# Optimization experiments

Measured on AMD Instinct MI355X. Metric: run time of the kernel, lower is better.

The kernel has to match this reference:

```python
import jax, jax.numpy as jnp
import numpy as np

N_NODES = 50000
N_EDGES = 800000
NFEAT = 128
NHID = 128
NCLASS = 10
N_GRAPHS = 256


def _segment_mean(vals, idx, num):
    # scatter-mean: sum then divide by count, count clamped to 1 (PyG 'mean' semantics)
    s = jax.ops.segment_sum(vals, idx, num_segments=num)
    c = jax.ops.segment_sum(jnp.ones((vals.shape[0], 1), vals.dtype), idx, num_segments=num)
    return s / jnp.maximum(c, 1.0)


def _graph_conv(x, src, dst, W_n, b_n, W_s):
    # gather x at source nodes, scatter-mean into destination nodes
    agg = _segment_mean(x[src], dst, x.shape[0])          # [N, C_in]
    return agg @ W_n.T + b_n + x @ W_s.T                  # [N, C_out]


def setup_inputs() -> dict:
    key = jax.random.key(0)
    ks = jax.random.split(key, 12)

    def lin_w(k, o, i):
        return (jax.random.uniform(k, (o, i), jnp.float32) * 2.0 - 1.0) / np.sqrt(i)

    x = jax.random.normal(ks[0], (N_NODES, NFEAT), jnp.float32)
    edge_index = jax.random.randint(ks[1], (2, N_EDGES), 0, N_NODES, dtype=jnp.int32)
    batch = jnp.sort(jax.random.randint(ks[2], (N_NODES,), 0, N_GRAPHS, dtype=jnp.int32))

    return {
        "x": x,
        "edge_index": edge_index,
        "batch": batch,
        "W1n": lin_w(ks[3], NHID, NFEAT), "b1": jnp.zeros((NHID,), jnp.float32), "W1s": lin_w(ks[4], NHID, NFEAT),
        "W2n": lin_w(ks[5], NHID, NHID), "b2": jnp.zeros((NHID,), jnp.float32), "W2s": lin_w(ks[6], NHID, NHID),
        "W3n": lin_w(ks[7], NHID, NHID), "b3": jnp.zeros((NHID,), jnp.float32), "W3s": lin_w(ks[8], NHID, NHID),
        "Wlin": lin_w(ks[9], NCLASS, NHID), "blin": jnp.zeros((NCLASS,), jnp.float32),
    }


def reference(x, edge_index, batch, W1n, b1, W1s, W2n, b2, W2s, W3n, b3, W3s, Wlin, blin):
    src, dst = edge_index[0], edge_index[1]
    h = jax.nn.relu(_graph_conv(x, src, dst, W1n, b1, W1s))
    h = jax.nn.relu(_graph_conv(h, src, dst, W2n, b2, W2s))
    h = jax.nn.relu(_graph_conv(h, src, dst, W3n, b3, W3s))
    g = _segment_mean(h, batch, N_GRAPHS)                 # global_mean_pool -> [G, NHID]
    # dropout is identity at inference
    logits = g @ Wlin.T + blin                            # [G, NCLASS]
    return jax.nn.log_softmax(logits, axis=1)
```

## Files before the change

kernel.cpp:

```cpp
#include <hip/hip_runtime.h>
#include <hip/hip_bf16.h>

#define NNODES 50000
#define NEDGES 800000
#define NFEAT 128
#define NHID 128
#define NCLASS 10
#define NGRAPHS 256

#define NB 391
#define HB 128

typedef __attribute__((ext_vector_type(8))) short short8;
typedef __attribute__((ext_vector_type(4))) short short4v;
typedef __attribute__((ext_vector_type(4))) float floatx4;

__device__ __forceinline__ float bf2f(unsigned short u) {
    union { unsigned i; float f; } c; c.i = ((unsigned)u) << 16; return c.f;
}
__device__ __forceinline__ unsigned short f2bf(float f) {
    union { float f; unsigned i; } c; c.f = f;
    unsigned x = c.i;
    unsigned r = (x + 0x7fffu + ((x >> 16) & 1u)) >> 16;
    return (unsigned short)r;
}
__device__ __forceinline__ float blo(unsigned v) { return bf2f((unsigned short)(v & 0xffffu)); }
__device__ __forceinline__ float bhi(unsigned v) { return bf2f((unsigned short)(v >> 16)); }

__device__ __forceinline__ void gload_lds16(const void* gsrc, void* ldst) {
    __builtin_amdgcn_global_load_lds(
        (const __attribute__((address_space(1))) void*)gsrc,
        (__attribute__((address_space(3))) void*)ldst, 16, 0, 0);
}

__global__ __launch_bounds__(256) void k_hist(const int* __restrict__ dst,
                                              int* __restrict__ hist) {
    __shared__ int lh[NB];
    int tid = threadIdx.x;
    for (int b = tid; b < NB; b += 256) lh[b] = 0;
    __syncthreads();
    for (int i = blockIdx.x * 256 + tid; i < NEDGES; i += HB * 256)
        atomicAdd(&lh[dst[i] >> 7], 1);
    __syncthreads();
    for (int b = tid; b < NB; b += 256) hist[b * HB + blockIdx.x] = lh[b];
}

__global__ __launch_bounds__(512) void k_scan2(const int* __restrict__ hist,
                                               int* __restrict__ base,
                                               int* __restrict__ boff,
                                               int* __restrict__ row_ptr,
                                               const int* __restrict__ batch,
                                               int* __restrict__ gstart) {
    __shared__ int tot[NB];
    int tid = threadIdx.x;
    int wid = tid >> 6, l = tid & 63;
    if (tid <= NGRAPHS) {
        int lo = 0, hi = NNODES;
        while (lo < hi) { int mid = (lo + hi) >> 1; if (batch[mid] < tid) lo = mid + 1; else hi = mid; }
        gstart[tid] = lo;
    }
    for (int q = wid; q < NB; q += 8) {
        int h0 = hist[q * HB + l];
        int h1 = hist[q * HB + 64 + l];
        int s0 = h0, s1 = h1;
        #pragma unroll
        for (int d = 1; d < 64; d <<= 1) {
            int y0 = __shfl_up(s0, d);
            int y1 = __shfl_up(s1, d);
            if (l >= d) { s0 += y0; s1 += y1; }
        }
        int t0 = __shfl(s0, 63);
        base[q * HB + l] = s0 - h0;
        base[q * HB + 64 + l] = s1 - h1 + t0;
        if (l == 63) tot[q] = t0 + s1;
    }
    __syncthreads();
    if (wid == 0) {
        int carry = 0;
        #pragma unroll
        for (int c = 0; c < (NB + 63) / 64; ++c) {
            int i = c * 64 + l;
            int v = (i < NB) ? tot[i] : 0;
            int s = v;
            #pragma unroll
            for (int d = 1; d < 64; d <<= 1) { int y = __shfl_up(s, d); if (l >= d) s += y; }
            if (i < NB) boff[i] = carry + s - v;
            carry += __shfl(s, 63);
        }
        if (l == 0) { boff[NB] = carry; row_ptr[NNODES] = carry; }
    }
}

__global__ __launch_bounds__(256) void k_scatter(const int* __restrict__ src,
                                                 const int* __restrict__ dst,
                                                 const int* __restrict__ base,
                                                 const int* __restrict__ boff,
                                                 unsigned* __restrict__ ebuf) {
    __shared__ int cur[NB];
    int tid = threadIdx.x;
    for (int b = tid; b < NB; b += 256) cur[b] = boff[b] + base[b * HB + blockIdx.x];
    __syncthreads();
    for (int i = blockIdx.x * 256 + tid; i < NEDGES; i += HB * 256) {
        int d = dst[i];
        int bin = d >> 7;
        int pos = atomicAdd(&cur[bin], 1);
        ebuf[pos] = (unsigned)src[i] | ((unsigned)(d & 127) << 16);
    }
}

__global__ __launch_bounds__(256) void k_bcsr(const unsigned* __restrict__ ebuf,
                                              const int* __restrict__ boff,
                                              int* __restrict__ row_ptr,
                                              int* __restrict__ esrc) {
    __shared__ int deg[128];
    __shared__ int curs[128];
    int tid = threadIdx.x;
    int b = blockIdx.x;
    int s = boff[b], e = boff[b + 1];
    if (tid < 128) deg[tid] = 0;
    __syncthreads();
    for (int i = s + tid; i < e; i += 256) atomicAdd(&deg[ebuf[i] >> 16], 1);
    __syncthreads();
    if (tid == 0) {
        int run = s;
        for (int i = 0; i < 128; ++i) { curs[i] = run; run += deg[i]; }
    }
    __syncthreads();
    if (tid < 128) {
        int node = b * 128 + tid;
        if (node < NNODES) row_ptr[node] = curs[tid];
    }
    __syncthreads();
    for (int i = s + tid; i < e; i += 256) {
        unsigned pk = ebuf[i];
        int pos = atomicAdd(&curs[pk >> 16], 1);
        esrc[pos] = (int)(pk & 0xffffu);
    }
}

__global__ void k_cvt(const float* __restrict__ x,
                      const float* __restrict__ w0, const float* __restrict__ w1,
                      const float* __restrict__ w2, const float* __restrict__ w3,
                      const float* __restrict__ w4, const float* __restrict__ w5,
                      unsigned short* __restrict__ xb, unsigned short* __restrict__ wb) {
    int gid = blockIdx.x * blockDim.x + threadIdx.x;
    const int NX4 = NNODES * NFEAT / 4;
    const floatx4* srcv;
    short4v* dstv;
    if (gid < NX4) {
        srcv = (const floatx4*)x + gid;
        dstv = (short4v*)xb + gid;
    } else {
        int j = gid - NX4;
        if (j >= 6 * 4096) return;
        int m = j >> 12;
        int o4 = j & 4095;
        const float* w = (m == 0) ? w0 : (m == 1) ? w1 : (m == 2) ? w2
                       : (m == 3) ? w3 : (m == 4) ? w4 : w5;
        srcv = (const floatx4*)w + o4;
        dstv = (short4v*)wb + (m * 4096 + o4);
    }
    floatx4 v = *srcv;
    short4v o;
    #pragma unroll
    for (int k = 0; k < 4; ++k) o[k] = (short)f2bf(v[k]);
    *dstv = o;
}

__global__ __launch_bounds__(512, 4) void k_layer(const unsigned short* __restrict__ feat,
                                                  const int* __restrict__ row_ptr,
                                                  const int* __restrict__ esrc,
                                                  const unsigned short* __restrict__ Bn,
                                                  const unsigned short* __restrict__ Bs,
                                                  const float* __restrict__ bias,
                                                  unsigned short* __restrict__ out) {
    __shared__ __align__(16) unsigned short ldsA[2][8192];
    int w = threadIdx.x >> 6;
    int l = threadIdx.x & 63;
    int r = l & 15;
    int gk = l >> 4;
    int m0 = blockIdx.x * 64;

    {
        int c = l & 15;
        #pragma unroll
        for (int is = 0; is < 2; ++is) {
            int row = is * 32 + (w << 2) + (l >> 4);
            int nrow = m0 + row; if (nrow >= NNODES) nrow = NNODES - 1;
            gload_lds16(feat + (size_t)nrow * 128 + ((c ^ (row & 15)) << 3),
                        &ldsA[1][(is * 32 + (w << 2)) * 128]);
        }
    }

    const unsigned* feat32 = (const unsigned*)feat;
    unsigned* A1 = (unsigned*)&ldsA[0][0];
    #pragma unroll 1
    for (int i = 0; i < 8; ++i) {
        int row = (w << 3) + i;
        int n = m0 + row;
        float a0 = 0.f, a1 = 0.f;
        int nb = 0;
        if (n < NNODES) {
            int beg = row_ptr[n];
            nb = row_ptr[n + 1] - beg;
            for (int base = 0; base < nb; base += 64) {
                int rem = nb - base;
                int cnt = rem < 64 ? rem : 64;
                int myidx = (l < cnt) ? esrc[beg + base + l] : 0;
                int j = 0;
                for (; j + 4 <= cnt; j += 4) {
                    int s0 = __shfl(myidx, j);
                    int s1 = __shfl(myidx, j + 1);
                    int s2 = __shfl(myidx, j + 2);
                    int s3 = __shfl(myidx, j + 3);
                    unsigned v0 = feat32[s0 * 64 + l];
                    unsigned v1 = feat32[s1 * 64 + l];
                    unsigned v2 = feat32[s2 * 64 + l];
                    unsigned v3 = feat32[s3 * 64 + l];
                    a0 += (blo(v0) + blo(v1)) + (blo(v2) + blo(v3));
                    a1 += (bhi(v0) + bhi(v1)) + (bhi(v2) + bhi(v3));
                }
                for (; j < cnt; ++j) {
                    int s0 = __shfl(myidx, j);
                    unsigned v0 = feat32[s0 * 64 + l];
                    a0 += blo(v0);
                    a1 += bhi(v0);
                }
            }
        }
        float inv = 1.0f / (float)max(nb, 1);
        unsigned o = ((unsigned)f2bf(a0 * inv)) | (((unsigned)f2bf(a1 * inv)) << 16);
        int c = l >> 2;
        A1[row * 64 + ((c ^ (row & 15)) << 2) + (l & 3)] = o;
    }

    short8 bf[8];
    #pragma unroll
    for (int kt = 0; kt < 8; ++kt) {
        const unsigned short* Bbase = (kt < 4 ? Bn : Bs);
        bf[kt] = *(const short8*)(Bbase + (w * 16 + r) * 128 + (kt & 3) * 32 + gk * 8);
    }
    int o = w * 16 + r;
    float bias_v = bias[o];

    __syncthreads();

    #pragma unroll
    for (int t = 0; t < 4; ++t) {
        short8 af[8];
        #pragma unroll
        for (int kt = 0; kt < 8; ++kt) {
            int half = kt >> 2;
            int Cr = ((((kt & 3) << 2) + gk) ^ r) << 3;
            af[kt] = *(const short8*)(&ldsA[half][(t * 16 + r) * 128 + Cr]);
        }
        floatx4 acc = {0.f, 0.f, 0.f, 0.f};
        #pragma unroll
        for (int kt = 0; kt < 8; ++kt)
            acc = __builtin_amdgcn_mfma_f32_16x16x32_bf16(af[kt], bf[kt], acc, 0, 0, 0);
        #pragma unroll
        for (int j = 0; j < 4; ++j) {
            int mrow = m0 + t * 16 + gk * 4 + j;
            if (mrow < NNODES) {
                float v = acc[j] + bias_v;
                v = v > 0.f ? v : 0.f;
                out[mrow * 128 + o] = f2bf(v);
            }
        }
    }
}

__global__ __launch_bounds__(256) void k_pool(const unsigned short* __restrict__ h,
                                              const int* __restrict__ gstart,
                                              float* __restrict__ part) {
    int g = blockIdx.x >> 3;
    int c = blockIdx.x & 7;
    int s = gstart[g], e = gstart[g + 1];
    int len = e - s;
    int cs = s + (len * c) / 8;
    int ce = s + (len * (c + 1)) / 8;
    int w = threadIdx.x >> 6;
    int l = threadIdx.x & 63;
    const unsigned* h32 = (const unsigned*)h;
    float a0 = 0.f, a1 = 0.f;
    for (int n = cs + w; n < ce; n += 4) {
        unsigned v = h32[n * 64 + l];
        a0 += blo(v);
        a1 += bhi(v);
    }
    __shared__ float red[4][128];
    red[w][2 * l] = a0;
    red[w][2 * l + 1] = a1;
    __syncthreads();
    if (w == 0) {
        float r0 = (red[0][2 * l] + red[1][2 * l]) + (red[2][2 * l] + red[3][2 * l]);
        float r1 = (red[0][2 * l + 1] + red[1][2 * l + 1]) + (red[2][2 * l + 1] + red[3][2 * l + 1]);
        float* dst = part + (size_t)(g * 8 + c) * 128;
        dst[2 * l] = r0;
        dst[2 * l + 1] = r1;
    }
}

__global__ __launch_bounds__(128) void k_head(const float* __restrict__ part,
                                              const int* __restrict__ gstart,
                                              const float* __restrict__ Wlin,
                                              const float* __restrict__ blin,
                                              float* __restrict__ out) {
    int gi = blockIdx.x;
    __shared__ float gl[128];
    __shared__ float lg[NCLASS];
    int t = threadIdx.x;
    float s = 0.f;
    #pragma unroll
    for (int c = 0; c < 8; ++c) s += part[(size_t)(gi * 8 + c) * 128 + t];
    int len = gstart[gi + 1] - gstart[gi];
    gl[t] = s / (float)max(len, 1);
    __syncthreads();
    if (t < NCLASS) {
        float a = blin[t];
        #pragma unroll 16
        for (int i = 0; i < 128; ++i) a += gl[i] * Wlin[t * 128 + i];
        lg[t] = a;
    }
    __syncthreads();
    if (t == 0) {
        float m = lg[0];
        for (int k = 1; k < NCLASS; ++k) m = fmaxf(m, lg[k]);
        float sum = 0.f;
        for (int k = 0; k < NCLASS; ++k) sum += expf(lg[k] - m);
        float ls = logf(sum) + m;
        for (int k = 0; k < NCLASS; ++k) out[gi * NCLASS + k] = lg[k] - ls;
    }
}

extern "C" void kernel_launch(void* const* d_in, const int* in_sizes, int n_in,
                              void* d_out, int out_size, void* d_ws, size_t ws_size,
                              hipStream_t stream) {
    const float* x    = (const float*)d_in[0];
    const int*   ei   = (const int*)d_in[1];
    const int*   src  = ei;
    const int*   dst  = ei + NEDGES;
    const int*   batch= (const int*)d_in[2];
    const float* W1n  = (const float*)d_in[3];
    const float* b1   = (const float*)d_in[4];
    const float* W1s  = (const float*)d_in[5];
    const float* W2n  = (const float*)d_in[6];
    const float* b2   = (const float*)d_in[7];
    const float* W2s  = (const float*)d_in[8];
    const float* W3n  = (const float*)d_in[9];
    const float* b3   = (const float*)d_in[10];
    const float* W3s  = (const float*)d_in[11];
    const float* Wlin = (const float*)d_in[12];
    const float* blin = (const float*)d_in[13];
    float* out = (float*)d_out;

    char* p = (char*)d_ws;
    auto alloc = [&](size_t bytes) -> void* {
        void* r = (void*)p;
        p += (bytes + 255) & ~(size_t)255;
        return r;
    };
    unsigned short* xb   = (unsigned short*)alloc((size_t)NNODES * NFEAT * 2);
    unsigned short* hA   = (unsigned short*)alloc((size_t)NNODES * NHID * 2);
    unsigned short* hB   = (unsigned short*)alloc((size_t)NNODES * NHID * 2);
    unsigned short* wb   = (unsigned short*)alloc((size_t)6 * 16384 * 2);
    int* hist    = (int*)alloc((size_t)NB * HB * 4);
    int* base    = (int*)alloc((size_t)NB * HB * 4);
    int* boff    = (int*)alloc((size_t)(NB + 1) * 4);
    int* row_ptr = (int*)alloc((size_t)(NNODES + 1) * 4);
    int* gstart  = (int*)alloc((size_t)(NGRAPHS + 1) * 4);
    unsigned* ebuf = (unsigned*)alloc((size_t)NEDGES * 4);
    int* esrc    = (int*)alloc((size_t)NEDGES * 4);
    float* part  = (float*)alloc((size_t)NGRAPHS * 8 * NHID * 4);

    k_hist<<<HB, 256, 0, stream>>>(dst, hist);
    k_scan2<<<1, 512, 0, stream>>>(hist, base, boff, row_ptr, batch, gstart);
    k_scatter<<<HB, 256, 0, stream>>>(src, dst, base, boff, ebuf);
    k_bcsr<<<NB, 256, 0, stream>>>(ebuf, boff, row_ptr, esrc);

    {
        int total4 = NNODES * NFEAT / 4 + 6 * 4096;
        k_cvt<<<(total4 + 255) / 256, 256, 0, stream>>>(x, W1n, W1s, W2n, W2s, W3n, W3s, xb, wb);
    }

    const int layerGrid = (NNODES + 63) / 64;

    k_layer<<<layerGrid, 512, 0, stream>>>(xb, row_ptr, esrc, wb + 0 * 16384, wb + 1 * 16384, b1, hA);
    k_layer<<<layerGrid, 512, 0, stream>>>(hA, row_ptr, esrc, wb + 2 * 16384, wb + 3 * 16384, b2, hB);
    k_layer<<<layerGrid, 512, 0, stream>>>(hB, row_ptr, esrc, wb + 4 * 16384, wb + 5 * 16384, b3, hA);

    k_pool<<<NGRAPHS * 8, 256, 0, stream>>>(hA, gstart, part);
    k_head<<<NGRAPHS, 128, 0, stream>>>(part, gstart, Wlin, blin, out);
}
```

Measured before the change: 209.5 us.

## Halve layer tile to 32 rows, prefetch next node's neighbor indices, unroll gather by 8

The fused aggregate+GEMM layer kernel now processes 32 nodes per 256-thread block instead of 64 per 512 threads, so each wave computes two output column stripes in the MFMA phase. The row_ptr values for a wave's 8 nodes are loaded once and shuffled, and the next node's edge indices are prefetched while the current node is gathered. The gather inner loop is unrolled to 8 loads in flight. The aim is to hide gather latency and improve load balance and occupancy, at the cost of loading B fragments for twice as many stripes per wave and higher register pressure.

```diff
diff --git a/kernel.cpp b/kernel.cpp
--- a/kernel.cpp
+++ b/kernel.cpp
@@ -167,86 +167,120 @@
     *dstv = o;
 }
 
-__global__ __launch_bounds__(512, 4) void k_layer(const unsigned short* __restrict__ feat,
+__global__ __launch_bounds__(256, 8) void k_layer(const unsigned short* __restrict__ feat,
                                                   const int* __restrict__ row_ptr,
                                                   const int* __restrict__ esrc,
                                                   const unsigned short* __restrict__ Bn,
                                                   const unsigned short* __restrict__ Bs,
                                                   const float* __restrict__ bias,
                                                   unsigned short* __restrict__ out) {
-    __shared__ __align__(16) unsigned short ldsA[2][8192];
+    __shared__ __align__(16) unsigned short ldsA[2][4096];
     int w = threadIdx.x >> 6;
     int l = threadIdx.x & 63;
     int r = l & 15;
     int gk = l >> 4;
-    int m0 = blockIdx.x * 64;
+    int m0 = blockIdx.x * 32;
 
     {
         int c = l & 15;
         #pragma unroll
         for (int is = 0; is < 2; ++is) {
-            int row = is * 32 + (w << 2) + (l >> 4);
+            int row = is * 16 + (w << 2) + (l >> 4);
             int nrow = m0 + row; if (nrow >= NNODES) nrow = NNODES - 1;
             gload_lds16(feat + (size_t)nrow * 128 + ((c ^ (row & 15)) << 3),
-                        &ldsA[1][(is * 32 + (w << 2)) * 128]);
+                        &ldsA[1][(is * 16 + (w << 2)) * 128]);
         }
     }
 
     const unsigned* feat32 = (const unsigned*)feat;
     unsigned* A1 = (unsigned*)&ldsA[0][0];
+    int n0 = m0 + (w << 3);
+    int rpl = row_ptr[min(n0 + l, NNODES)];
+    int beg = __shfl(rpl, 0);
+    int nb  = __shfl(rpl, 1) - beg;
+    int myidx = (l < (nb < 64 ? nb : 64)) ? esrc[beg + l] : 0;
+
     #pragma unroll 1
     for (int i = 0; i < 8; ++i) {
+        int nbeg = 0, nnb = 0, nmy = 0;
+        if (i < 7) {
+            nbeg = __shfl(rpl, i + 1);
+            nnb  = __shfl(rpl, i + 2) - nbeg;
+            nmy = (l < (nnb < 64 ? nnb : 64)) ? esrc[nbeg + l] : 0;
+        }
+        float a0 = 0.f, a1 = 0.f;
+        for (int base = 0; base < nb; base += 64) {
+            int rem = nb - base;
+            int cnt = rem < 64 ? rem : 64;
+            int idxv = (base == 0) ? myidx
+                     : ((l < cnt) ? esrc[beg + base + l] : 0);
+            int j = 0;
+            for (; j + 8 <= cnt; j += 8) {
+                int s0 = __shfl(idxv, j);
+                int s1 = __shfl(idxv, j + 1);
+                int s2 = __shfl(idxv, j + 2);
+                int s3 = __shfl(idxv, j + 3);
+                int s4 = __shfl(idxv, j + 4);
+                int s5 = __shfl(idxv, j + 5);
+                int s6 = __shfl(idxv, j + 6);
+                int s7 = __shfl(idxv, j + 7);
+                unsigned v0 = feat32[s0 * 64 + l];
+                unsigned v1 = feat32[s1 * 64 + l];
+                unsigned v2 = feat32[s2 * 64 + l];
+                unsigned v3 = feat32[s3 * 64 + l];
+                unsigned v4 = feat32[s4 * 64 + l];
+                unsigned v5 = feat32[s5 * 64 + l];
+                unsigned v6 = feat32[s6 * 64 + l];
+                unsigned v7 = feat32[s7 * 64 + l];
+                a0 += ((blo(v0) + blo(v1)) + (blo(v2) + blo(v3)))
+                    + ((blo(v4) + blo(v5)) + (blo(v6) + blo(v7)));
+                a1 += ((bhi(v0) + bhi(v1)) + (bhi(v2) + bhi(v3)))
+                    + ((bhi(v4) + bhi(v5)) + (bhi(v6) + bhi(v7)));
+            }
+            for (; j + 4 <= cnt; j += 4) {
+                int s0 = __shfl(idxv, j);
+                int s1 = __shfl(idxv, j + 1);
+                int s2 = __shfl(idxv, j + 2);
+                int s3 = __shfl(idxv, j + 3);
+                unsigned v0 = feat32[s0 * 64 + l];
+                unsigned v1 = feat32[s1 * 64 + l];
+                unsigned v2 = feat32[s2 * 64 + l];
+                unsigned v3 = feat32[s3 * 64 + l];
+                a0 += (blo(v0) + blo(v1)) + (blo(v2) + blo(v3));
+                a1 += (bhi(v0) + bhi(v1)) + (bhi(v2) + bhi(v3));
+            }
+            for (; j < cnt; ++j) {
+                int s0 = __shfl(idxv, j);
+                unsigned v0 = feat32[s0 * 64 + l];
+                a0 += blo(v0);
+                a1 += bhi(v0);
+            }
+        }
         int row = (w << 3) + i;
-        int n = m0 + row;
-        float a0 = 0.f, a1 = 0.f;
-        int nb = 0;
-        if (n < NNODES) {
-            int beg = row_ptr[n];
-            nb = row_ptr[n + 1] - beg;
-            for (int base = 0; base < nb; base += 64) {
-                int rem = nb - base;
-                int cnt = rem < 64 ? rem : 64;
-                int myidx = (l < cnt) ? esrc[beg + base + l] : 0;
-                int j = 0;
-                for (; j + 4 <= cnt; j += 4) {
-                    int s0 = __shfl(myidx, j);
-                    int s1 = __shfl(myidx, j + 1);
-                    int s2 = __shfl(myidx, j + 2);
-                    int s3 = __shfl(myidx, j + 3);
-                    unsigned v0 = feat32[s0 * 64 + l];
-                    unsigned v1 = feat32[s1 * 64 + l];
-                    unsigned v2 = feat32[s2 * 64 + l];
-                    unsigned v3 = feat32[s3 * 64 + l];
-                    a0 += (blo(v0) + blo(v1)) + (blo(v2) + blo(v3));
-                    a1 += (bhi(v0) + bhi(v1)) + (bhi(v2) + bhi(v3));
-                }
-                for (; j < cnt; ++j) {
-                    int s0 = __shfl(myidx, j);
-                    unsigned v0 = feat32[s0 * 64 + l];
-                    a0 += blo(v0);
-                    a1 += bhi(v0);
-                }
-            }
-        }
         float inv = 1.0f / (float)max(nb, 1);
         unsigned o = ((unsigned)f2bf(a0 * inv)) | (((unsigned)f2bf(a1 * inv)) << 16);
         int c = l >> 2;
         A1[row * 64 + ((c ^ (row & 15)) << 2) + (l & 3)] = o;
-    }
-
-    short8 bf[8];
+        beg = nbeg; nb = nnb; myidx = nmy;
+    }
+
+    short8 bf[2][8];
+    float bias_v[2];
     #pragma unroll
-    for (int kt = 0; kt < 8; ++kt) {
-        const unsigned short* Bbase = (kt < 4 ? Bn : Bs);
-        bf[kt] = *(const short8*)(Bbase + (w * 16 + r) * 128 + (kt & 3) * 32 + gk * 8);
-    }
-    int o = w * 16 + r;
-    float bias_v = bias[o];
+    for (int s = 0; s < 2; ++s) {
+        int stripe = (w << 1) + s;
+        #pragma unroll
+        for (int kt = 0; kt < 8; ++kt) {
+            const unsigned short* Bbase = (kt < 4 ? Bn : Bs);
+            bf[s][kt] = *(const short8*)(Bbase + (stripe * 16 + r) * 128 + (kt & 3) * 32 + gk * 8);
+        }
+        bias_v[s] = bias[stripe * 16 + r];
+    }
 
     __syncthreads();
 
     #pragma unroll
-    for (int t = 0; t < 4; ++t) {
+    for (int t = 0; t < 2; ++t) {
         short8 af[8];
         #pragma unroll
         for (int kt = 0; kt < 8; ++kt) {
@@ -254,17 +288,21 @@
             int Cr = ((((kt & 3) << 2) + gk) ^ r) << 3;
             af[kt] = *(const short8*)(&ldsA[half][(t * 16 + r) * 128 + Cr]);
         }
-        floatx4 acc = {0.f, 0.f, 0.f, 0.f};
-        #pragma unroll
-        for (int kt = 0; kt < 8; ++kt)
-            acc = __builtin_amdgcn_mfma_f32_16x16x32_bf16(af[kt], bf[kt], acc, 0, 0, 0);
-        #pragma unroll
-        for (int j = 0; j < 4; ++j) {
-            int mrow = m0 + t * 16 + gk * 4 + j;
-            if (mrow < NNODES) {
-                float v = acc[j] + bias_v;
-                v = v > 0.f ? v : 0.f;
-                out[mrow * 128 + o] = f2bf(v);
+        #pragma unroll
+        for (int s = 0; s < 2; ++s) {
+            floatx4 acc = {0.f, 0.f, 0.f, 0.f};
+            #pragma unroll
+            for (int kt = 0; kt < 8; ++kt)
+                acc = __builtin_amdgcn_mfma_f32_16x16x32_bf16(af[kt], bf[s][kt], acc, 0, 0, 0);
+            int o = ((w << 1) + s) * 16 + r;
+            #pragma unroll
+            for (int j = 0; j < 4; ++j) {
+                int mrow = m0 + t * 16 + gk * 4 + j;
+                if (mrow < NNODES) {
+                    float v = acc[j] + bias_v[s];
+                    v = v > 0.f ? v : 0.f;
+                    out[mrow * 128 + o] = f2bf(v);
+                }
             }
         }
     }
@@ -383,11 +421,11 @@
         k_cvt<<<(total4 + 255) / 256, 256, 0, stream>>>(x, W1n, W1s, W2n, W2s, W3n, W3s, xb, wb);
     }
 
-    const int layerGrid = (NNODES + 63) / 64;
-
-    k_layer<<<layerGrid, 512, 0, stream>>>(xb, row_ptr, esrc, wb + 0 * 16384, wb + 1 * 16384, b1, hA);
-    k_layer<<<layerGrid, 512, 0, stream>>>(hA, row_ptr, esrc, wb + 2 * 16384, wb + 3 * 16384, b2, hB);
-    k_layer<<<layerGrid, 512, 0, stream>>>(hB, row_ptr, esrc, wb + 4 * 16384, wb + 5 * 16384, b3, hA);
+    const int layerGrid = (NNODES + 31) / 32;
+
+    k_layer<<<layerGrid, 256, 0, stream>>>(xb, row_ptr, esrc, wb + 0 * 16384, wb + 1 * 16384, b1, hA);
+    k_layer<<<layerGrid, 256, 0, stream>>>(hA, row_ptr, esrc, wb + 2 * 16384, wb + 3 * 16384, b2, hB);
+    k_layer<<<layerGrid, 256, 0, stream>>>(hB, row_ptr, esrc, wb + 4 * 16384, wb + 5 * 16384, b3, hA);
 
     k_pool<<<NGRAPHS * 8, 256, 0, stream>>>(hA, gstart, part);
     k_head<<<NGRAPHS, 128, 0, stream>>>(part, gstart, Wlin, blin, out);
```

Result: slower. 300.2 us (+43.3%).
